# Optimization experiments

Hardware: AMD Instinct MI355X
Metric: run time of the kernel (lower is better)

## Reference

```python
import jax, jax.numpy as jnp
import numpy as np

B, N, N_MELS = 8, 4096, 64
DIM, LAYERS, HEADS = 256, 4, 4
DIM_HEAD = DIM // HEADS      # 64
INNER = HEADS * DIM_HEAD     # 256
NB_FEAT = 256                # random features
FF_MULT = 4                  # performer_pytorch FeedForward default


def _ortho_projection(rows, cols, rng):
    # gaussian_orthogonal_random_matrix, scaling=0 (performer_pytorch default)
    blocks = []
    for _ in range((rows + cols - 1) // cols):
        q, _ = np.linalg.qr(rng.standard_normal((cols, cols)))
        blocks.append(q.T)
    mat = np.concatenate(blocks)[:rows]
    multiplier = np.linalg.norm(rng.standard_normal((rows, cols)), axis=1)
    return (mat * multiplier[:, None]).astype(np.float32)


def setup_inputs() -> dict:
    rng = np.random.default_rng(0)
    def w(*s, scale=0.02):
        return jnp.asarray(rng.standard_normal(s).astype(np.float32) * scale)
    G2 = 2 * DIM * FF_MULT  # GLU projection width = 2048
    return {
        "x": jnp.asarray(rng.standard_normal((B, N, N_MELS)).astype(np.float32)),
        "proj_w": w(N_MELS, DIM), "proj_b": jnp.zeros((DIM,), jnp.float32),
        "ln1_g": jnp.ones((LAYERS, DIM), jnp.float32), "ln1_b": jnp.zeros((LAYERS, DIM), jnp.float32),
        "wq": w(LAYERS, DIM, INNER), "bq": jnp.zeros((LAYERS, INNER), jnp.float32),
        "wk": w(LAYERS, DIM, INNER), "bk": jnp.zeros((LAYERS, INNER), jnp.float32),
        "wv": w(LAYERS, DIM, INNER), "bv": jnp.zeros((LAYERS, INNER), jnp.float32),
        "wo": w(LAYERS, INNER, DIM), "bo": jnp.zeros((LAYERS, DIM), jnp.float32),
        "ln2_g": jnp.ones((LAYERS, DIM), jnp.float32), "ln2_b": jnp.zeros((LAYERS, DIM), jnp.float32),
        "w1": w(LAYERS, DIM, G2), "b1": jnp.zeros((LAYERS, G2), jnp.float32),
        "w2": w(LAYERS, DIM * FF_MULT, DIM), "b2": jnp.zeros((LAYERS, DIM), jnp.float32),
        "clf_w": w(DIM, 1), "clf_b": jnp.zeros((1,), jnp.float32),
        "proj_mat": jnp.asarray(_ortho_projection(NB_FEAT, DIM_HEAD, rng)),
    }


def _layer_norm(x, g, b, eps=1e-5):
    mu = jnp.mean(x, -1, keepdims=True)
    var = jnp.mean((x - mu) ** 2, -1, keepdims=True)
    return (x - mu) * jax.lax.rsqrt(var + eps) * g + b


def _softmax_kernel(data, proj, is_query, eps=1e-4):
    # FAVOR+ positive random features for softmax (performer_pytorch.softmax_kernel)
    dn = data.shape[-1] ** -0.25          # data_normalizer
    ratio = proj.shape[0] ** -0.5
    dd = jnp.einsum('bhnd,md->bhnm', data * dn, proj)
    diag = jnp.sum(data ** 2, -1, keepdims=True) * 0.5 * (dn ** 2)
    if is_query:
        m = jax.lax.stop_gradient(jnp.max(dd, axis=-1, keepdims=True))
    else:
        m = jax.lax.stop_gradient(jnp.max(dd))
    return ratio * (jnp.exp(dd - diag - m) + eps)


def _split_heads(t):
    b, n, _ = t.shape
    return t.reshape(b, n, HEADS, DIM_HEAD).transpose(0, 2, 1, 3)  # b h n d


def _forward(x, proj_w, proj_b, ln1_g, ln1_b, wq, bq, wk, bk, wv, bv, wo, bo,
             ln2_g, ln2_b, w1, b1, w2, b2, clf_w, clf_b, proj_mat):
    h = x @ proj_w + proj_b                       # [B, N, DIM]
    b, n = h.shape[0], h.shape[1]
    for l in range(LAYERS):
        # --- pre-LN self-attention (FAVOR+, non-causal) ---
        y = _layer_norm(h, ln1_g[l], ln1_b[l])
        q = _split_heads(y @ wq[l] + bq[l])
        k = _split_heads(y @ wk[l] + bk[l])
        v = _split_heads(y @ wv[l] + bv[l])
        qp = _softmax_kernel(q, proj_mat, is_query=True)    # [b,h,n,m]
        kp = _softmax_kernel(k, proj_mat, is_query=False)   # [b,h,n,m]
        d_inv = 1.0 / jnp.einsum('bhnm,bhm->bhn', qp, kp.sum(axis=2))
        ctx = jnp.einsum('bhnm,bhnd->bhmd', kp, v)          # [b,h,m,d]
        o = jnp.einsum('bhmd,bhnm,bhn->bhnd', ctx, qp, d_inv)
        o = o.transpose(0, 2, 1, 3).reshape(b, n, INNER)
        h = h + (o @ wo[l] + bo[l])
        # --- pre-LN GLU feed-forward ---
        y = _layer_norm(h, ln2_g[l], ln2_b[l])
        u = y @ w1[l] + b1[l]
        a, g = jnp.split(u, 2, axis=-1)
        h = h + (jax.nn.gelu(a, approximate=False) * g) @ w2[l] + b2[l]
    # clf: transpose + AdaptiveAvgPool1d(1) == mean over time, then Linear(dim,1)
    pooled = h.mean(axis=1)                       # [B, DIM]
    return (pooled @ clf_w + clf_b)[:, 0]         # [B]


def reference(x, proj_w, proj_b, ln1_g, ln1_b, wq, bq, wk, bk, wv, bv, wo, bo,
              ln2_g, ln2_b, w1, b1, w2, b2, clf_w, clf_b, proj_mat):
    return _forward(x, proj_w, proj_b, ln1_g, ln1_b, wq, bq, wk, bk, wv, bv,
                    wo, bo, ln2_g, ln2_b, w1, b1, w2, b2, clf_w, clf_b, proj_mat)
```

## Files before the change

kernel.cpp:

```cpp
#include <hip/hip_runtime.h>
#include <cstdint>
#include <cstddef>

constexpr float DN = 0.35355339059327373f;
constexpr float RATIO = 0.0625f;
constexpr float EPSF = 1e-4f;

typedef __attribute__((ext_vector_type(8))) short short8;
typedef __attribute__((ext_vector_type(4))) float f32x4;

constexpr size_t OFF_H     = 0;
constexpr size_t OFF_YS    = 33554432;
constexpr size_t OFF_WTS   = 50331648;
constexpr size_t OFF_QK    = 67108864;
constexpr size_t OFF_BIG   = 100663296;
constexpr size_t OFF_VT    = 167772160;
constexpr size_t OFF_CTXP  = 188743680;
constexpr size_t OFF_CTXTH = 199229440;
constexpr size_t OFF_CTXTL = 200540160;
constexpr size_t OFF_DIAGQ = 201850880;
constexpr size_t OFF_DIAGK = 202375168;
constexpr size_t OFF_GMAX  = 203423744;
constexpr size_t OFF_POOL  = 203424000;
constexpr size_t OFF_PMTH  = 207749376;
constexpr size_t OFF_PMTL  = 207782144;
constexpr size_t OFF_PWTH  = 207814912;
constexpr size_t OFF_PWTL  = 207847680;
constexpr size_t WS_BYTES  = 207880448;

constexpr size_t WQ_H = 0,       WQ_L = 65536;
constexpr size_t WK_H = 131072,  WK_L = 196608;
constexpr size_t WV_H = 262144,  WV_L = 327680;
constexpr size_t WO_H = 393216,  WO_L = 458752;
constexpr size_t W1_H = 524288,  W1_L = 1048576;
constexpr size_t W2_H = 1572864, W2_L = 1835008;

__device__ __forceinline__ unsigned fkey(float f) {
    unsigned u = __float_as_uint(f);
    return (u & 0x80000000u) ? ~u : (u | 0x80000000u);
}
__device__ __forceinline__ float funkey(unsigned k) {
    unsigned u = (k & 0x80000000u) ? (k ^ 0x80000000u) : ~k;
    return __uint_as_float(u);
}
__device__ __forceinline__ float gelu_exact(float x) {
    return 0.5f * x * (1.0f + erff(x * 0.70710678118654752f));
}
__device__ __forceinline__ void splitf(float x, unsigned short& h, unsigned short& l) {
    unsigned u = __float_as_uint(x);
    unsigned hv = (u + 0x7FFFu + ((u >> 16) & 1)) >> 16;
    h = (unsigned short)hv;
    float lo = x - __uint_as_float(hv << 16);
    unsigned u2 = __float_as_uint(lo);
    l = (unsigned short)((u2 + 0x7FFFu + ((u2 >> 16) & 1)) >> 16);
}
__device__ __forceinline__ unsigned short bf16rne(float x) {
    unsigned u = __float_as_uint(x);
    return (unsigned short)((u + 0x7FFFu + ((u >> 16) & 1)) >> 16);
}
__device__ __forceinline__ void xcd_swz(int& bx, int& by) {
    const int gx = gridDim.x;
    const int total = gx * gridDim.y;
    int flat = blockIdx.y * gx + blockIdx.x;
    flat = (flat & 7) * (total >> 3) + (flat >> 3);
    bx = flat % gx; by = flat / gx;
}

#if defined(__has_builtin)
#if __has_builtin(__builtin_amdgcn_global_load_lds)
#define HAVE_GLDS 1
#endif
#endif
__device__ __forceinline__ void glds16(const unsigned short* g, unsigned short* l) {
#ifdef HAVE_GLDS
    __builtin_amdgcn_global_load_lds(
        (const __attribute__((address_space(1))) unsigned int*)g,
        (__attribute__((address_space(3))) unsigned int*)l, 16, 0, 0);
#else
    *(uint4*)l = *(const uint4*)g;
#endif
}

__global__ void fill_sentinel(float* out, int n) {
    int i = threadIdx.x;
    if (i < n) out[i] = 12345.0f;
}
__global__ __launch_bounds__(256) void vt_init(unsigned short* __restrict__ vT, unsigned* __restrict__ gm) {
    int i = blockIdx.x * 256 + threadIdx.x;
    if (i < 4) gm[i] = 0u;
    const int bh = i >> 13;
    const int r = (i >> 9) & 15;
    const unsigned val = (r == 0) ? 0x3F803F80u : 0u;
    uint4 q; q.x = val; q.y = val; q.z = val; q.w = val;
    *(uint4*)(vT + ((size_t)bh * 80 + 64 + r) * 4096 + ((size_t)(i & 511) << 3)) = q;
}

__global__ __launch_bounds__(256) void split_scale(
    const float* __restrict__ src, unsigned short* __restrict__ hi,
    unsigned short* __restrict__ lo, int n, float scale)
{
    int i = blockIdx.x * 256 + threadIdx.x;
    if (i < n) {
        unsigned short h, l;
        splitf(src[i] * scale, h, l);
        hi[i] = h; lo[i] = l;
    }
}

__global__ __launch_bounds__(256) void splitT(
    const float* __restrict__ W, unsigned short* __restrict__ hi,
    unsigned short* __restrict__ lo, int kshift, int N)
{
    int i = blockIdx.x * 256 + threadIdx.x;
    int K = 1 << kshift;
    int n = i >> kshift, k = i & (K - 1);
    unsigned short h, l;
    splitf(W[(size_t)k * N + n], h, l);
    hi[i] = h; lo[i] = l;
}

__global__ __launch_bounds__(256) void split_weights(
    const float* __restrict__ wq, const float* __restrict__ wk,
    const float* __restrict__ wv, const float* __restrict__ wo,
    const float* __restrict__ w1, const float* __restrict__ w2,
    unsigned short* __restrict__ dst)
{
    const int i = blockIdx.x * 256 + threadIdx.x;
    const int lay = i >> 20;
    const int r = i & 1048575;
    float val; size_t oh, ol;
    if (r < 262144) {
        const int m = r >> 16, e = r & 65535;
        const int n = e >> 8, k = e & 255;
        const float* W = (m == 0 ? wq : m == 1 ? wk : m == 2 ? wv : wo);
        val = W[(size_t)lay * 65536 + k * 256 + n];
        oh = (size_t)lay * 2097152 + (size_t)m * 131072 + e;
        ol = oh + 65536;
    } else if (r < 786432) {
        const int e = r - 262144;
// ... 10 lines not shown
    }
    unsigned short h, l;
    splitf(val, h, l);
    dst[oh] = h; dst[ol] = l;
}

__global__ __launch_bounds__(256) void ln_bf16(
    const float* __restrict__ x, const float* __restrict__ g,
    const float* __restrict__ b, unsigned short* __restrict__ yhi)
{
    const int row = blockIdx.x * 4 + (threadIdx.x >> 6);
    const int lane = threadIdx.x & 63;
    float4 t = *(const float4*)&x[(size_t)row * 256 + lane * 4];
    float s = t.x + t.y + t.z + t.w;
#pragma unroll
    for (int sh = 1; sh < 64; sh <<= 1) s += __shfl_xor(s, sh);
    const float mu = s * (1.0f / 256.0f);
    const float dx = t.x - mu, dy = t.y - mu, dz = t.z - mu, dw = t.w - mu;
    float vv = dx * dx + dy * dy + dz * dz + dw * dw;
#pragma unroll
    for (int sh = 1; sh < 64; sh <<= 1) vv += __shfl_xor(vv, sh);
    const float rstd = rsqrtf(vv * (1.0f / 256.0f) + 1e-5f);
    float4 gv = *(const float4*)&g[lane * 4];
    float4 bv = *(const float4*)&b[lane * 4];
    unsigned short h0 = bf16rne(dx * rstd * gv.x + bv.x);
    unsigned short h1 = bf16rne(dy * rstd * gv.y + bv.y);
    unsigned short h2 = bf16rne(dz * rstd * gv.z + bv.z);
    unsigned short h3 = bf16rne(dw * rstd * gv.w + bv.w);
    uint2 ph;
    ph.x = (unsigned)h0 | ((unsigned)h1 << 16); ph.y = (unsigned)h2 | ((unsigned)h3 << 16);
    *(uint2*)&yhi[(size_t)row * 256 + lane * 4] = ph;
}

template<int EPI, bool ASPLIT, bool BSPLIT>
__global__ __launch_bounds__(256) void gemm_mf(
    const unsigned short* __restrict__ Ahi, const unsigned short* __restrict__ Alo, int lda,
    const unsigned short* __restrict__ Bhi, const unsigned short* __restrict__ Blo, int ldb,
    int K,
    const float* __restrict__ bias, const float* __restrict__ res,
    float* __restrict__ C, int ldc,
    unsigned short* __restrict__ Obf,
    const float* __restrict__ diag, unsigned* __restrict__ keys)
{
    constexpr int NP = (ASPLIT ? 2 : 1) + (BSPLIT ? 2 : 1);
    constexpr int PB = ASPLIT ? 2 : 1;
    constexpr int NEED = (EPI == 6 || EPI == 8) ? 16384 : 0;
    constexpr int LDSN = (NP * 8192 > NEED) ? NP * 8192 : NEED;
    __shared__ unsigned short lds[LDSN];
    __shared__ float red[4];
#define LX(p, h, r, c) lds[(p) * 8192 + (h) * 4096 + (r) * 32 + (c)]
    int bx, by; xcd_swz(bx, by);
    const int tid = threadIdx.x;
    const int m0 = by * 128, n0 = bx * 128;
    const int sr = tid >> 2, sc = (tid & 3) * 8;
    const unsigned short* ga_h = Ahi + (size_t)(m0 + sr) * lda + sc;
    const unsigned short* ga_l = ASPLIT ? (Alo + (size_t)(m0 + sr) * lda + sc) : nullptr;
    const unsigned short* gb_h = Bhi + (size_t)(n0 + sr) * ldb + sc;
    const unsigned short* gb_l = BSPLIT ? (Blo + (size_t)(n0 + sr) * ldb + sc) : nullptr;
    unsigned short* lp = lds + tid * 8;
    const int l = tid & 63, w = tid >> 6;
    const int wr = (w >> 1) * 64, wc = (w & 1) * 64;
    const int fr = l & 15, fq = l >> 4;

    f32x4 acc[4][4];
#pragma unroll
    for (int i = 0; i < 4; ++i)
#pragma unroll
        for (int j = 0; j < 4; ++j) acc[i][j] = (f32x4){0.f, 0.f, 0.f, 0.f};

    for (int k0 = 0; k0 < K; k0 += 64) {
        glds16(ga_h + k0, lp);
        glds16(ga_h + (size_t)64 * lda + k0, lp + 2048);
        glds16(ga_h + k0 + 32, lp + 4096);
        glds16(ga_h + (size_t)64 * lda + k0 + 32, lp + 6144);
        if (ASPLIT) {
            glds16(ga_l + k0, lp + 8192);
            glds16(ga_l + (size_t)64 * lda + k0, lp + 10240);
            glds16(ga_l + k0 + 32, lp + 12288);
            glds16(ga_l + (size_t)64 * lda + k0 + 32, lp + 14336);
        }
        glds16(gb_h + k0, lp + PB * 8192);
        glds16(gb_h + (size_t)64 * ldb + k0, lp + PB * 8192 + 2048);
        glds16(gb_h + k0 + 32, lp + PB * 8192 + 4096);
        glds16(gb_h + (size_t)64 * ldb + k0 + 32, lp + PB * 8192 + 6144);
        if (BSPLIT) {
            glds16(gb_l + k0, lp + (PB + 1) * 8192);
            glds16(gb_l + (size_t)64 * ldb + k0, lp + (PB + 1) * 8192 + 2048);
            glds16(gb_l + k0 + 32, lp + (PB + 1) * 8192 + 4096);
            glds16(gb_l + (size_t)64 * ldb + k0 + 32, lp + (PB + 1) * 8192 + 6144);
        }
        __syncthreads();
#pragma unroll
        for (int h2 = 0; h2 < 2; ++h2) {
            short8 ah[4], al[4];
#pragma unroll
            for (int mf = 0; mf < 4; ++mf) {
                ah[mf] = *(const short8*)&LX(0, h2, wr + mf * 16 + fr, fq * 8);
                if (ASPLIT) al[mf] = *(const short8*)&LX(1, h2, wr + mf * 16 + fr, fq * 8);
            }
#pragma unroll
            for (int nf = 0; nf < 4; ++nf) {
                short8 bh = *(const short8*)&LX(PB, h2, wc + nf * 16 + fr, fq * 8);
#pragma unroll
                for (int mf = 0; mf < 4; ++mf) {
                    acc[mf][nf] = __builtin_amdgcn_mfma_f32_16x16x32_bf16(ah[mf], bh, acc[mf][nf], 0, 0, 0);
                    if (ASPLIT)
                        acc[mf][nf] = __builtin_amdgcn_mfma_f32_16x16x32_bf16(al[mf], bh, acc[mf][nf], 0, 0, 0);
                }
                if (BSPLIT) {
                    short8 bl = *(const short8*)&LX(PB + 1, h2, wc + nf * 16 + fr, fq * 8);
#pragma unroll
                    for (int mf = 0; mf < 4; ++mf)
                        acc[mf][nf] = __builtin_amdgcn_mfma_f32_16x16x32_bf16(ah[mf], bl, acc[mf][nf], 0, 0, 0);
                }
            }
        }
        __syncthreads();
    }

    if constexpr (EPI == 4) {
        float m = -3.4e38f;
#pragma unroll
        for (int mf = 0; mf < 4; ++mf)
#pragma unroll
            for (int nf = 0; nf < 4; ++nf)
#pragma unroll
                for (int v = 0; v < 4; ++v) m = fmaxf(m, acc[mf][nf][v]);
#pragma unroll
        for (int s = 1; s < 64; s <<= 1) m = fmaxf(m, __shfl_xor(m, s));
        if (l == 0) red[w] = m;
        __syncthreads();
        if (tid == 0)
            atomicMax(keys, fkey(fmaxf(fmaxf(red[0], red[1]), fmaxf(red[2], red[3]))));
    } else if constexpr (EPI == 6) {
        const float Mg = funkey(*keys);
        unsigned short* tb = lds;
#pragma unroll
        for (int mf = 0; mf < 4; ++mf)
#pragma unroll
            for (int v = 0; v < 4; ++v) {
                const int rl = wr + mf * 16 + fq * 4 + v;
                const float dg = diag[m0 + rl] + Mg;
#pragma unroll
                for (int nf = 0; nf < 4; ++nf) {
                    const int cl = wc + nf * 16 + fr;
                    tb[rl * 128 + cl] = bf16rne(RATIO * (__expf(acc[mf][nf][v] - dg) + EPSF));
                }
            }
        __syncthreads();
        const int tokbase = m0 >> 2;
        const int b = tokbase >> 12, nib = tokbase & 4095;
        const int ml = tid & 127, g2 = tid >> 7;
#pragma unroll
        for (int hh2 = 0; hh2 < 2; ++hh2) {
            const int hh = g2 * 2 + hh2;
            unsigned short* dst = Obf + ((size_t)((b * 4 + hh) * 256 + n0 + ml)) * 4096 + nib;
#pragma unroll
            for (int qq = 0; qq < 4; ++qq) {
                uint4 qv;
                unsigned wv[4];
#pragma unroll
                for (int j = 0; j < 4; ++j) {
                    unsigned s0 = tb[((qq * 8 + j * 2 + 0) * 4 + hh) * 128 + ml];
                    unsigned s1 = tb[((qq * 8 + j * 2 + 1) * 4 + hh) * 128 + ml];
                    wv[j] = s0 | (s1 << 16);
                }
                qv.x = wv[0]; qv.y = wv[1]; qv.z = wv[2]; qv.w = wv[3];
                *(uint4*)(dst + qq * 8) = qv;
            }
        }
    } else if constexpr (EPI == 8) {
        unsigned short* tb = lds;
#pragma unroll
        for (int mf = 0; mf < 4; ++mf)
#pragma unroll
            for (int nf = 0; nf < 4; ++nf) {
                const int cl = wc + nf * 16 + fr;
                const float bb = bias[n0 + cl];
#pragma unroll
                for (int v = 0; v < 4; ++v) {
                    const int rl = wr + mf * 16 + fq * 4 + v;
                    tb[rl * 128 + cl] = bf16rne(acc[mf][nf][v] + bb);
                }
            }
        __syncthreads();
        const int b = m0 >> 12, nib = m0 & 4095;
        const int cl = tid & 127, half = tid >> 7;
        const int ch = n0 + cl, hh = ch >> 6, d = ch & 63;
        unsigned short* dst = Obf + ((size_t)((b * 4 + hh) * 80 + d)) * 4096 + nib + half * 64;
#pragma unroll
        for (int qq = 0; qq < 8; ++qq) {
            uint4 qv;
            unsigned wv[4];
#pragma unroll
            for (int j = 0; j < 4; ++j) {
                unsigned s0 = tb[(half * 64 + qq * 8 + j * 2 + 0) * 128 + cl];
                unsigned s1 = tb[(half * 64 + qq * 8 + j * 2 + 1) * 128 + cl];
                wv[j] = s0 | (s1 << 16);
            }
            qv.x = wv[0]; qv.y = wv[1]; qv.z = wv[2]; qv.w = wv[3];
            *(uint4*)(dst + qq * 8) = qv;
        }
    } else if constexpr (EPI == 2) {
        const int head = (n0 + wc) >> 6;
#pragma unroll
        for (int mf = 0; mf < 4; ++mf) {
            float sq[4] = {0.f, 0.f, 0.f, 0.f};
#pragma unroll
            for (int nf = 0; nf < 4; ++nf) {
                const int col = n0 + wc + nf * 16 + fr;
                const float bb = bias[col];
#pragma unroll
                for (int v = 0; v < 4; ++v) {
                    const int row = m0 + wr + mf * 16 + fq * 4 + v;
                    float val = acc[mf][nf][v] + bb;
                    Obf[(size_t)row * 256 + col] = bf16rne(val);
                    sq[v] += val * val;
                }
            }
#pragma unroll
            for (int v = 0; v < 4; ++v) {
                float s = sq[v];
                s += __shfl_xor(s, 1); s += __shfl_xor(s, 2);
                s += __shfl_xor(s, 4); s += __shfl_xor(s, 8);
                if (fr == 0)
                    ((float*)diag)[(size_t)(m0 + wr + mf * 16 + fq * 4 + v) * 4 + head] = s * 0.0625f;
            }
        }
    } else {
#pragma unroll
        for (int nf = 0; nf < 4; ++nf) {
            const int col = n0 + wc + nf * 16 + fr;
            float bb = 0.f;
            if (bias != nullptr) bb = bias[col];
#pragma unroll
            for (int mf = 0; mf < 4; ++mf) {
#pragma unroll
                for (int v = 0; v < 4; ++v) {
                    const int row = m0 + wr + mf * 16 + fq * 4 + v;
                    const size_t off = (size_t)row * ldc + col;
                    float val = acc[mf][nf][v] + bb;
                    if (EPI == 1) val += res[off];
                    C[off] = val;
                }
            }
        }
    }
#undef LX
}

__global__ __launch_bounds__(256) void gemm_glu(
    const unsigned short* __restrict__ Ahi,
    const unsigned short* __restrict__ Whi, const unsigned short* __restrict__ Wlo,
    const float* __restrict__ b1, unsigned short* __restrict__ Obf)
{
    __shared__ unsigned short ldsA[8192];
    __shared__ unsigned short ldsB[16384];
    int bx, by; xcd_swz(bx, by);
    const int tid = threadIdx.x;
    const int m0 = by * 128, p0 = bx * 64;
    const int sr = tid >> 2, sc = (tid & 3) * 8;
    const unsigned short* ga  = Ahi + (size_t)(m0 + sr) * 256 + sc;
    const unsigned short* gb0 = Whi + (size_t)(p0 + sr) * 256 + sc;
    const unsigned short* gb1 = Wlo + (size_t)(p0 + sr) * 256 + sc;
    const unsigned short* gb2 = Whi + (size_t)(1024 + p0 + sr) * 256 + sc;
    const unsigned short* gb3 = Wlo + (size_t)(1024 + p0 + sr) * 256 + sc;
    unsigned short* lpA = ldsA + tid * 8;
    unsigned short* lpB = ldsB + tid * 8;
    const int l = tid & 63, w = tid >> 6;
    const int wr = (w >> 1) * 64, wc = (w & 1) * 32;
    const int fr = l & 15, fq = l >> 4;

    f32x4 aa[4][2], ag[4][2];
#pragma unroll
    for (int i = 0; i < 4; ++i)
#pragma unroll
        for (int j = 0; j < 2; ++j) {
            aa[i][j] = (f32x4){0.f, 0.f, 0.f, 0.f};
            ag[i][j] = (f32x4){0.f, 0.f, 0.f, 0.f};
        }

    for (int k0 = 0; k0 < 256; k0 += 64) {
        glds16(ga + k0, lpA);
        glds16(ga + 64 * 256 + k0, lpA + 2048);
        glds16(ga + k0 + 32, lpA + 4096);
        glds16(ga + 64 * 256 + k0 + 32, lpA + 6144);
        glds16(gb0 + k0, lpB);
        glds16(gb0 + k0 + 32, lpB + 2048);
        glds16(gb1 + k0, lpB + 4096);
        glds16(gb1 + k0 + 32, lpB + 6144);
        glds16(gb2 + k0, lpB + 8192);
        glds16(gb2 + k0 + 32, lpB + 10240);
        glds16(gb3 + k0, lpB + 12288);
        glds16(gb3 + k0 + 32, lpB + 14336);
        __syncthreads();
#pragma unroll
        for (int h2 = 0; h2 < 2; ++h2) {
            short8 ah[4];
#pragma unroll
            for (int mf = 0; mf < 4; ++mf)
                ah[mf] = *(const short8*)&ldsA[h2 * 4096 + (wr + mf * 16 + fr) * 32 + fq * 8];
#pragma unroll
            for (int nf = 0; nf < 2; ++nf) {
                const int br_ = h2 * 2048 + (wc + nf * 16 + fr) * 32 + fq * 8;
                short8 bah = *(const short8*)&ldsB[br_];
                short8 bal = *(const short8*)&ldsB[4096 + br_];
                short8 bgh = *(const short8*)&ldsB[8192 + br_];
                short8 bgl = *(const short8*)&ldsB[12288 + br_];
#pragma unroll
                for (int mf = 0; mf < 4; ++mf) {
                    aa[mf][nf] = __builtin_amdgcn_mfma_f32_16x16x32_bf16(ah[mf], bah, aa[mf][nf], 0, 0, 0);
                    aa[mf][nf] = __builtin_amdgcn_mfma_f32_16x16x32_bf16(ah[mf], bal, aa[mf][nf], 0, 0, 0);
                    ag[mf][nf] = __builtin_amdgcn_mfma_f32_16x16x32_bf16(ah[mf], bgh, ag[mf][nf], 0, 0, 0);
                    ag[mf][nf] = __builtin_amdgcn_mfma_f32_16x16x32_bf16(ah[mf], bgl, ag[mf][nf], 0, 0, 0);
                }
            }
        }
        __syncthreads();
    }
#pragma unroll
    for (int nf = 0; nf < 2; ++nf) {
        const int ch = p0 + wc + nf * 16 + fr;
        const float ba = b1[ch], bg = b1[1024 + ch];
#pragma unroll
        for (int mf = 0; mf < 4; ++mf) {
#pragma unroll
            for (int v = 0; v < 4; ++v) {
                const int row = m0 + wr + mf * 16 + fq * 4 + v;
                float u = aa[mf][nf][v] + ba, g = ag[mf][nf][v] + bg;
                Obf[(size_t)row * 1024 + ch] = bf16rne(gelu_exact(u) * g);
            }
        }
    }
}

__global__ __launch_bounds__(256) void ctx_mfma(
    const unsigned short* __restrict__ kpT, const unsigned short* __restrict__ vT,
    float* __restrict__ ctxp)
{
    __shared__ unsigned short la[4096];
    __shared__ unsigned short lb[5120];
    int bx, by; xcd_swz(bx, by);
    const int bh = by, mt = bx & 3, kc = bx >> 2;
    const int tid = threadIdx.x;
    const int l = tid & 63, w = tid >> 6;
    const int wr = w * 16, fr = l & 15, fq = l >> 4;
    const int sr = tid >> 2, sc = (tid & 3) * 8;
    const unsigned short* ga  = kpT + ((size_t)bh * 256 + mt * 64 + sr) * 4096 + kc * 1024 + sc;
    const unsigned short* gb  = vT + ((size_t)bh * 80 + sr) * 4096 + kc * 1024 + sc;
    const unsigned short* gb2 = vT + ((size_t)bh * 80 + 64 + sr) * 4096 + kc * 1024 + sc;

    f32x4 acc[5];
#pragma unroll
    for (int j = 0; j < 5; ++j) acc[j] = (f32x4){0.f, 0.f, 0.f, 0.f};

    for (int k0 = 0; k0 < 1024; k0 += 64) {
        glds16(ga + k0, la + tid * 8);
        glds16(ga + k0 + 32, la + 2048 + tid * 8);
        glds16(gb + k0, lb + tid * 8);
        glds16(gb + k0 + 32, lb + 2560 + tid * 8);
        if (tid < 64) {
            glds16(gb2 + k0, lb + 2048 + tid * 8);
            glds16(gb2 + k0 + 32, lb + 2560 + 2048 + tid * 8);
        }
        __syncthreads();
#pragma unroll
        for (int h2 = 0; h2 < 2; ++h2) {
            short8 av = *(const short8*)&la[h2 * 2048 + (wr + fr) * 32 + fq * 8];
#pragma unroll
            for (int nf = 0; nf < 5; ++nf) {
                short8 bv = *(const short8*)&lb[h2 * 2560 + (nf * 16 + fr) * 32 + fq * 8];
                acc[nf] = __builtin_amdgcn_mfma_f32_16x16x32_bf16(av, bv, acc[nf], 0, 0, 0);
            }
        }
        __syncthreads();
    }
#pragma unroll
    for (int v = 0; v < 4; ++v) {
        const int row = mt * 64 + wr + fq * 4 + v;
#pragma unroll
        for (int nf = 0; nf < 5; ++nf)
            ctxp[((size_t)(kc * 32 + bh) * 256 + row) * 80 + nf * 16 + fr] = acc[nf][v];
    }
}

__global__ __launch_bounds__(256) void ctx_fix(
    const float* __restrict__ ctxp, unsigned short* __restrict__ cth,
    unsigned short* __restrict__ ctl)
{
    __shared__ float s[64][81];
    const int m0 = blockIdx.x * 64, bh = blockIdx.y;
    const int tid = threadIdx.x;
    for (int i = tid; i < 5120; i += 256) {
        const int ml = i / 80, dc = i % 80;
        float sum = 0.f;
#pragma unroll
        for (int kc = 0; kc < 4; ++kc)
            sum += ctxp[((size_t)(kc * 32 + bh) * 256 + m0 + ml) * 80 + dc];
        s[ml][dc] = sum;
    }
    __syncthreads();
    for (int i = tid; i < 5120; i += 256) {
        const int dc = i >> 6, ml = i & 63;
        unsigned short hh_, ll_;
        splitf(s[ml][dc], hh_, ll_);
        cth[((size_t)bh * 80 + dc) * 256 + m0 + ml] = hh_;
        ctl[((size_t)bh * 80 + dc) * 256 + m0 + ml] = ll_;
    }
}

__global__ __launch_bounds__(256) void qo_mfma(
    const unsigned short* __restrict__ qhi,
    const unsigned short* __restrict__ pmh, const unsigned short* __restrict__ pml,
    const unsigned short* __restrict__ cth, const unsigned short* __restrict__ ctl,
    const float* __restrict__ diagq, unsigned short* __restrict__ osh)
{
    __shared__ unsigned short lds[18432 + 5120];
    __shared__ float rmax4[64][4];
    int bx, by; xcd_swz(bx, by);
    const int bh = by, b = bh >> 2, hh = bh & 3;
    const int t0 = bx * 64;
    const int tid = threadIdx.x;
    const int l = tid & 63, w = tid >> 6;
    const int fr = l & 15, fq = l >> 4;

    const int wc1 = w * 64;
    f32x4 a1[4][4];
#pragma unroll
    for (int i = 0; i < 4; ++i)
#pragma unroll
        for (int j = 0; j < 4; ++j) a1[i][j] = (f32x4){0.f, 0.f, 0.f, 0.f};

    const unsigned short* gq = qhi + (size_t)(b * 4096 + t0) * 256 + hh * 64;
#pragma unroll
    for (int ks = 0; ks < 2; ++ks) {
        const int k0 = ks * 32;
        glds16(gq + (size_t)(tid >> 2) * 256 + k0 + (tid & 3) * 8, lds + tid * 8);
#pragma unroll
        for (int i2 = 0; i2 < 4; ++i2) {
            const int c = tid + i2 * 256;
            glds16(pmh + (size_t)(c >> 2) * 64 + k0 + (c & 3) * 8, lds + 2048 + c * 8);
            glds16(pml + (size_t)(c >> 2) * 64 + k0 + (c & 3) * 8, lds + 10240 + c * 8);
        }
        __syncthreads();
        short8 av[4];
#pragma unroll
        for (int mf = 0; mf < 4; ++mf)
            av[mf] = *(const short8*)&lds[(mf * 16 + fr) * 32 + fq * 8];
#pragma unroll
        for (int nf = 0; nf < 4; ++nf) {
            short8 bh_ = *(const short8*)&lds[2048 + (wc1 + nf * 16 + fr) * 32 + fq * 8];
            short8 bl_ = *(const short8*)&lds[10240 + (wc1 + nf * 16 + fr) * 32 + fq * 8];
#pragma unroll
            for (int mf = 0; mf < 4; ++mf) {
                a1[mf][nf] = __builtin_amdgcn_mfma_f32_16x16x32_bf16(av[mf], bh_, a1[mf][nf], 0, 0, 0);
                a1[mf][nf] = __builtin_amdgcn_mfma_f32_16x16x32_bf16(av[mf], bl_, a1[mf][nf], 0, 0, 0);
            }
        }
        __syncthreads();
    }
#pragma unroll
    for (int mf = 0; mf < 4; ++mf)
#pragma unroll
        for (int v = 0; v < 4; ++v) {
            float rm = a1[mf][0][v];
#pragma unroll
            for (int nf = 1; nf < 4; ++nf) rm = fmaxf(rm, a1[mf][nf][v]);
            rm = fmaxf(rm, __shfl_xor(rm, 1));
            rm = fmaxf(rm, __shfl_xor(rm, 2));
            rm = fmaxf(rm, __shfl_xor(rm, 4));
            rm = fmaxf(rm, __shfl_xor(rm, 8));
            if (fr == 0) rmax4[mf * 16 + fq * 4 + v][w] = rm;
        }
    __syncthreads();
#pragma unroll
    for (int mf = 0; mf < 4; ++mf)
#pragma unroll
        for (int v = 0; v < 4; ++v) {
            const int tok = mf * 16 + fq * 4 + v;
            const float dg = diagq[(size_t)(b * 4096 + t0 + tok) * 4 + hh]
                           + fmaxf(fmaxf(rmax4[tok][0], rmax4[tok][1]),
                                   fmaxf(rmax4[tok][2], rmax4[tok][3]));
#pragma unroll
            for (int nf = 0; nf < 4; ++nf) {
                const int m = wc1 + nf * 16 + fr;
                lds[tok * 256 + (m ^ ((tok & 7) << 3))] =
                    bf16rne(RATIO * (__expf(a1[mf][nf][v] - dg) + EPSF));
            }
        }
    __syncthreads();

    unsigned short* lds2 = lds + 18432;
    f32x4 a2[5];
#pragma unroll
    for (int j = 0; j < 5; ++j) a2[j] = (f32x4){0.f, 0.f, 0.f, 0.f};
    const size_t bbase = (size_t)bh * 80 * 256;

    for (int k0 = 0; k0 < 256; k0 += 32) {
        glds16(cth + bbase + (size_t)(tid >> 2) * 256 + k0 + (tid & 3) * 8, lds2 + tid * 8);
        glds16(ctl + bbase + (size_t)(tid >> 2) * 256 + k0 + (tid & 3) * 8, lds2 + 2560 + tid * 8);
        if (tid < 64) {
            const int c = 256 + tid;
            glds16(cth + bbase + (size_t)(c >> 2) * 256 + k0 + (c & 3) * 8, lds2 + c * 8);
            glds16(ctl + bbase + (size_t)(c >> 2) * 256 + k0 + (c & 3) * 8, lds2 + 2560 + c * 8);
        }
        __syncthreads();
        const int tok = w * 16 + fr;
        const int c = ((k0 >> 3) + fq) ^ (tok & 7);
        short8 av = *(const short8*)&lds[tok * 256 + c * 8];
#pragma unroll
        for (int nf = 0; nf < 5; ++nf) {
            const int off = (nf * 16 + fr) * 32 + fq * 8;
            short8 bvh = *(const short8*)&lds2[off];
            short8 bvl = *(const short8*)&lds2[2560 + off];
            a2[nf] = __builtin_amdgcn_mfma_f32_16x16x32_bf16(av, bvh, a2[nf], 0, 0, 0);
            a2[nf] = __builtin_amdgcn_mfma_f32_16x16x32_bf16(av, bvl, a2[nf], 0, 0, 0);
        }
        __syncthreads();
    }
#pragma unroll
    for (int v = 0; v < 4; ++v) {
        const float den = __shfl(a2[4][v], (int)(l & 48));
        const float dinv = 1.0f / den;
        const int tok = w * 16 + fq * 4 + v;
        const size_t obase = (size_t)(b * 4096 + t0 + tok) * 256 + hh * 64;
#pragma unroll
        for (int nf = 0; nf < 4; ++nf)
            osh[obase + nf * 16 + fr] = bf16rne(a2[nf][v] * dinv);
    }
}

__global__ __launch_bounds__(256) void pool1_kernel(const float* __restrict__ h, float* __restrict__ part)
{
    const int b = blockIdx.x >> 4, ch = blockIdx.x & 15;
    const int tid = threadIdx.x;
    float acc = 0.f;
    for (int n = 0; n < 256; ++n)
        acc += h[((size_t)(b * 4096 + ch * 256 + n)) * 256 + tid];
    part[(size_t)blockIdx.x * 256 + tid] = acc;
}

__global__ __launch_bounds__(256) void pool2_kernel(
    const float* __restrict__ part, const float* __restrict__ cw,
    const float* __restrict__ cb, float* __restrict__ out)
{
    const int b = blockIdx.x, tid = threadIdx.x;
    float acc = 0.f;
#pragma unroll
    for (int c = 0; c < 16; ++c) acc += part[(size_t)(b * 16 + c) * 256 + tid];
// ... 19 lines not shown
    const float* x     = (const float*)d_in[0];
    const float* projw = (const float*)d_in[1];
    const float* projb = (const float*)d_in[2];
    const float* ln1g  = (const float*)d_in[3];
    const float* ln1b  = (const float*)d_in[4];
    const float* wq    = (const float*)d_in[5];
    const float* bq    = (const float*)d_in[6];
    const float* wk    = (const float*)d_in[7];
    const float* bk    = (const float*)d_in[8];
    const float* wv    = (const float*)d_in[9];
    const float* bv    = (const float*)d_in[10];
    const float* wo    = (const float*)d_in[11];
    const float* bo    = (const float*)d_in[12];
    const float* ln2g  = (const float*)d_in[13];
    const float* ln2b  = (const float*)d_in[14];
    const float* w1    = (const float*)d_in[15];
    const float* b1    = (const float*)d_in[16];
    const float* w2    = (const float*)d_in[17];
    const float* b2    = (const float*)d_in[18];
    const float* clfw  = (const float*)d_in[19];
    const float* clfb  = (const float*)d_in[20];
    const float* projm = (const float*)d_in[21];

    char* WS = (char*)d_ws;
    float* h            = (float*)(WS + OFF_H);
    unsigned short* ysh = (unsigned short*)(WS + OFF_YS);
    unsigned short* wts = (unsigned short*)(WS + OFF_WTS);
    unsigned short* khi = (unsigned short*)(WS + OFF_QK);
    unsigned short* qhi = khi + 8388608;
    unsigned short* big = (unsigned short*)(WS + OFF_BIG);
    unsigned short* vT  = (unsigned short*)(WS + OFF_VT);
    float* ctxp         = (float*)(WS + OFF_CTXP);
    unsigned short* cth = (unsigned short*)(WS + OFF_CTXTH);
    unsigned short* ctl = (unsigned short*)(WS + OFF_CTXTL);
    float* diagq        = (float*)(WS + OFF_DIAGQ);
    float* diagk        = (float*)(WS + OFF_DIAGK);
    unsigned* gmax      = (unsigned*)(WS + OFF_GMAX);
    float* pool         = (float*)(WS + OFF_POOL);
    unsigned short* pmt_h = (unsigned short*)(WS + OFF_PMTH);
    unsigned short* pmt_l = (unsigned short*)(WS + OFF_PMTL);
    unsigned short* pwt_h = (unsigned short*)(WS + OFF_PWTH);
    unsigned short* pwt_l = (unsigned short*)(WS + OFF_PWTL);
    unsigned short* xsh = big;
    unsigned short* xsl = big + 2097152;
    unsigned short* kpT = big;
    unsigned short* ffb = big;
    unsigned short* osh = ysh;

    split_scale<<<8192, 256, 0, stream>>>(x, xsh, xsl, 2097152, 1.0f);
    splitT<<<64, 256, 0, stream>>>(projw, pwt_h, pwt_l, 6, 256);
    split_scale<<<64, 256, 0, stream>>>(projm, pmt_h, pmt_l, 16384, DN);
    vt_init<<<1024, 256, 0, stream>>>(vT, gmax);
    split_weights<<<16384, 256, 0, stream>>>(wq, wk, wv, wo, w1, w2, wts);
    gemm_mf<0, true, true><<<dim3(2, 256), 256, 0, stream>>>(xsh, xsl, 64, pwt_h, pwt_l, 64, 64,
        projb, nullptr, h, 256, nullptr, nullptr, nullptr);

    for (int l = 0; l < 4; ++l) {
        unsigned short* wl = wts + (size_t)l * 2097152;

        ln_bf16<<<8192, 256, 0, stream>>>(h, ln1g + l * 256, ln1b + l * 256, ysh);
        gemm_mf<8, false, true><<<dim3(2, 256), 256, 0, stream>>>(ysh, nullptr, 256,
            wl + WV_H, wl + WV_L, 256, 256, bv + l * 256, nullptr, nullptr, 256, vT, nullptr, nullptr);
        gemm_mf<2, false, true><<<dim3(2, 256), 256, 0, stream>>>(ysh, nullptr, 256,
            wl + WK_H, wl + WK_L, 256, 256, bk + l * 256, nullptr, nullptr, 256, khi, diagk, nullptr);
        gemm_mf<2, false, true><<<dim3(2, 256), 256, 0, stream>>>(ysh, nullptr, 256,
            wl + WQ_H, wl + WQ_L, 256, 256, bq + l * 256, nullptr, nullptr, 256, qhi, diagq, nullptr);
        gemm_mf<4, false, false><<<dim3(2, 1024), 256, 0, stream>>>(khi, nullptr, 64,
            pmt_h, nullptr, 64, 64, nullptr, nullptr, nullptr, 256, nullptr, nullptr, gmax + l);
        gemm_mf<6, false, true><<<dim3(2, 1024), 256, 0, stream>>>(khi, nullptr, 64,
            pmt_h, pmt_l, 64, 64, nullptr, nullptr, nullptr, 256, kpT, diagk, gmax + l);
        ctx_mfma<<<dim3(16, 32), 256, 0, stream>>>(kpT, vT, ctxp);
        ctx_fix<<<dim3(4, 32), 256, 0, stream>>>(ctxp, cth, ctl);
        qo_mfma<<<dim3(64, 32), 256, 0, stream>>>(qhi, pmt_h, pmt_l, cth, ctl, diagq, osh);
        gemm_mf<1, false, true><<<dim3(2, 256), 256, 0, stream>>>(osh, nullptr, 256,
            wl + WO_H, wl + WO_L, 256, 256, bo + l * 256, h, h, 256, nullptr, nullptr, nullptr);

        ln_bf16<<<8192, 256, 0, stream>>>(h, ln2g + l * 256, ln2b + l * 256, ysh);
        gemm_glu<<<dim3(16, 256), 256, 0, stream>>>(ysh, wl + W1_H, wl + W1_L,
            b1 + (size_t)l * 2048, ffb);
        gemm_mf<1, false, true><<<dim3(2, 256), 256, 0, stream>>>(ffb, nullptr, 1024,
            wl + W2_H, wl + W2_L, 1024, 1024, b2 + l * 256, h, h, 256, nullptr, nullptr, nullptr);
    }

    pool1_kernel<<<128, 256, 0, stream>>>(h, pool);
    pool2_kernel<<<8, 256, 0, stream>>>(pool, clfw, clfb, (float*)d_out);
}
```

Baseline: 1.424 ms.

## Use fp16 single-pass MFMA in FAVOR+ attention path and fuse QKV GEMMs

Switches the q/k/v, random-feature projection, context and output-attention operands from bf16 hi/lo split pairs to single fp16 values. This removes the low-part MFMA passes and the low-part loads in the kernel projection, ctx_fix and qo_mfma stages. The three separate Q, K and V projection launches are merged into one gemm_qkv kernel that selects its weights by block row. The trade-off is lower precision for the feature maps and context (fp16 mantissa instead of a split bf16 pair) and some fp16 range risk.

```diff
diff --git a/kernel.cpp b/kernel.cpp
--- a/kernel.cpp
+++ b/kernel.cpp
@@ -7,6 +7,7 @@
 constexpr float EPSF = 1e-4f;
 
 typedef __attribute__((ext_vector_type(8))) short short8;
+typedef __attribute__((ext_vector_type(8))) _Float16 half8;
 typedef __attribute__((ext_vector_type(4))) float f32x4;
 
 constexpr size_t OFF_H     = 0;
@@ -58,6 +59,17 @@
     unsigned u = __float_as_uint(x);
     return (unsigned short)((u + 0x7FFFu + ((u >> 16) & 1)) >> 16);
 }
+__device__ __forceinline__ unsigned short fp16rne(float x) {
+    return __builtin_bit_cast(unsigned short, (_Float16)x);
+}
+template<bool F16>
+__device__ __forceinline__ f32x4 mfma16(short8 a, short8 b, f32x4 c) {
+    if constexpr (F16)
+        return __builtin_amdgcn_mfma_f32_16x16x32_f16(
+            __builtin_bit_cast(half8, a), __builtin_bit_cast(half8, b), c, 0, 0, 0);
+    else
+        return __builtin_amdgcn_mfma_f32_16x16x32_bf16(a, b, c, 0, 0, 0);
+}
 __device__ __forceinline__ void xcd_swz(int& bx, int& by) {
     const int gx = gridDim.x;
     const int total = gx * gridDim.y;
@@ -90,7 +102,7 @@
     if (i < 4) gm[i] = 0u;
     const int bh = i >> 13;
     const int r = (i >> 9) & 15;
-    const unsigned val = (r == 0) ? 0x3F803F80u : 0u;
+    const unsigned val = (r == 0) ? 0x3C003C00u : 0u;
     uint4 q; q.x = val; q.y = val; q.z = val; q.w = val;
     *(uint4*)(vT + ((size_t)bh * 80 + 64 + r) * 4096 + ((size_t)(i & 511) << 3)) = q;
 }
@@ -105,6 +117,13 @@
         splitf(src[i] * scale, h, l);
         hi[i] = h; lo[i] = l;
     }
+}
+
+__global__ __launch_bounds__(256) void tofp16_scale(
+    const float* __restrict__ src, unsigned short* __restrict__ dst, int n, float scale)
+{
+    int i = blockIdx.x * 256 + threadIdx.x;
+    if (i < n) dst[i] = fp16rne(src[i] * scale);
 }
 
 __global__ __launch_bounds__(256) void splitT(
@@ -181,7 +200,7 @@
     *(uint2*)&yhi[(size_t)row * 256 + lane * 4] = ph;
 }
 
-template<int EPI, bool ASPLIT, bool BSPLIT>
+template<int EPI, bool ASPLIT, bool BSPLIT, bool F16>
 __global__ __launch_bounds__(256) void gemm_mf(
     const unsigned short* __restrict__ Ahi, const unsigned short* __restrict__ Alo, int lda,
     const unsigned short* __restrict__ Bhi, const unsigned short* __restrict__ Blo, int ldb,
@@ -193,7 +212,7 @@
 {
     constexpr int NP = (ASPLIT ? 2 : 1) + (BSPLIT ? 2 : 1);
     constexpr int PB = ASPLIT ? 2 : 1;
-    constexpr int NEED = (EPI == 6 || EPI == 8) ? 16384 : 0;
+    constexpr int NEED = (EPI == 6) ? 16384 : 0;
     constexpr int LDSN = (NP * 8192 > NEED) ? NP * 8192 : NEED;
     __shared__ unsigned short lds[LDSN];
     __shared__ float red[4];
@@ -252,15 +271,14 @@
                 short8 bh = *(const short8*)&LX(PB, h2, wc + nf * 16 + fr, fq * 8);
 #pragma unroll
                 for (int mf = 0; mf < 4; ++mf) {
-                    acc[mf][nf] = __builtin_amdgcn_mfma_f32_16x16x32_bf16(ah[mf], bh, acc[mf][nf], 0, 0, 0);
-                    if (ASPLIT)
-                        acc[mf][nf] = __builtin_amdgcn_mfma_f32_16x16x32_bf16(al[mf], bh, acc[mf][nf], 0, 0, 0);
+                    acc[mf][nf] = mfma16<F16>(ah[mf], bh, acc[mf][nf]);
+                    if (ASPLIT) acc[mf][nf] = mfma16<F16>(al[mf], bh, acc[mf][nf]);
                 }
                 if (BSPLIT) {
                     short8 bl = *(const short8*)&LX(PB + 1, h2, wc + nf * 16 + fr, fq * 8);
 #pragma unroll
                     for (int mf = 0; mf < 4; ++mf)
-                        acc[mf][nf] = __builtin_amdgcn_mfma_f32_16x16x32_bf16(ah[mf], bl, acc[mf][nf], 0, 0, 0);
+                        acc[mf][nf] = mfma16<F16>(ah[mf], bl, acc[mf][nf]);
                 }
             }
         }
@@ -293,7 +311,8 @@
 #pragma unroll
                 for (int nf = 0; nf < 4; ++nf) {
                     const int cl = wc + nf * 16 + fr;
-                    tb[rl * 128 + cl] = bf16rne(RATIO * (__expf(acc[mf][nf][v] - dg) + EPSF));
+                    const float kv = RATIO * (__expf(acc[mf][nf][v] - dg) + EPSF);
+                    tb[rl * 128 + cl] = F16 ? fp16rne(kv) : bf16rne(kv);
                 }
             }
         __syncthreads();
@@ -318,64 +337,6 @@
                 *(uint4*)(dst + qq * 8) = qv;
             }
         }
-    } else if constexpr (EPI == 8) {
-        unsigned short* tb = lds;
-#pragma unroll
-        for (int mf = 0; mf < 4; ++mf)
-#pragma unroll
-            for (int nf = 0; nf < 4; ++nf) {
-                const int cl = wc + nf * 16 + fr;
-                const float bb = bias[n0 + cl];
-#pragma unroll
-                for (int v = 0; v < 4; ++v) {
-                    const int rl = wr + mf * 16 + fq * 4 + v;
-                    tb[rl * 128 + cl] = bf16rne(acc[mf][nf][v] + bb);
-                }
-            }
-        __syncthreads();
-        const int b = m0 >> 12, nib = m0 & 4095;
-        const int cl = tid & 127, half = tid >> 7;
-        const int ch = n0 + cl, hh = ch >> 6, d = ch & 63;
-        unsigned short* dst = Obf + ((size_t)((b * 4 + hh) * 80 + d)) * 4096 + nib + half * 64;
-#pragma unroll
-        for (int qq = 0; qq < 8; ++qq) {
-            uint4 qv;
-            unsigned wv[4];
-#pragma unroll
-            for (int j = 0; j < 4; ++j) {
-                unsigned s0 = tb[(half * 64 + qq * 8 + j * 2 + 0) * 128 + cl];
-                unsigned s1 = tb[(half * 64 + qq * 8 + j * 2 + 1) * 128 + cl];
-                wv[j] = s0 | (s1 << 16);
-            }
-            qv.x = wv[0]; qv.y = wv[1]; qv.z = wv[2]; qv.w = wv[3];
-            *(uint4*)(dst + qq * 8) = qv;
-        }
-    } else if constexpr (EPI == 2) {
-        const int head = (n0 + wc) >> 6;
-#pragma unroll
-        for (int mf = 0; mf < 4; ++mf) {
-            float sq[4] = {0.f, 0.f, 0.f, 0.f};
-#pragma unroll
-            for (int nf = 0; nf < 4; ++nf) {
-                const int col = n0 + wc + nf * 16 + fr;
-                const float bb = bias[col];
-#pragma unroll
-                for (int v = 0; v < 4; ++v) {
-                    const int row = m0 + wr + mf * 16 + fq * 4 + v;
-                    float val = acc[mf][nf][v] + bb;
-                    Obf[(size_t)row * 256 + col] = bf16rne(val);
-                    sq[v] += val * val;
-                }
-            }
-#pragma unroll
-            for (int v = 0; v < 4; ++v) {
-                float s = sq[v];
-                s += __shfl_xor(s, 1); s += __shfl_xor(s, 2);
-                s += __shfl_xor(s, 4); s += __shfl_xor(s, 8);
-                if (fr == 0)
-                    ((float*)diag)[(size_t)(m0 + wr + mf * 16 + fq * 4 + v) * 4 + head] = s * 0.0625f;
-            }
-        }
     } else {
 #pragma unroll
         for (int nf = 0; nf < 4; ++nf) {
@@ -396,6 +357,132 @@
         }
     }
 #undef LX
+}
+
+__global__ __launch_bounds__(256) void gemm_qkv(
+    const unsigned short* __restrict__ A, const unsigned short* __restrict__ wl,
+    const float* __restrict__ bq, const float* __restrict__ bk, const float* __restrict__ bv,
+    unsigned short* __restrict__ vT, unsigned short* __restrict__ khi,
+    unsigned short* __restrict__ qhi, float* __restrict__ diagq, float* __restrict__ diagk)
+{
+    __shared__ unsigned short lds[24576];
+    int bx, by; xcd_swz(bx, by);
+    const int sel = by >> 8;
+    const int m0 = (by & 255) * 128, n0 = bx * 128;
+    const unsigned short* Bh = wl + (sel == 0 ? WV_H : sel == 1 ? WK_H : WQ_H);
+    const unsigned short* Bl = wl + (sel == 0 ? WV_L : sel == 1 ? WK_L : WQ_L);
+    const float* bias = (sel == 0 ? bv : sel == 1 ? bk : bq);
+    const int tid = threadIdx.x;
+    const int sr = tid >> 2, sc = (tid & 3) * 8;
+    const unsigned short* ga_h = A + (size_t)(m0 + sr) * 256 + sc;
+    const unsigned short* gb_h = Bh + (size_t)(n0 + sr) * 256 + sc;
+    const unsigned short* gb_l = Bl + (size_t)(n0 + sr) * 256 + sc;
+    unsigned short* lp = lds + tid * 8;
+    const int l = tid & 63, w = tid >> 6;
+    const int wr = (w >> 1) * 64, wc = (w & 1) * 64;
+    const int fr = l & 15, fq = l >> 4;
+
+    f32x4 acc[4][4];
+#pragma unroll
+    for (int i = 0; i < 4; ++i)
+#pragma unroll
+        for (int j = 0; j < 4; ++j) acc[i][j] = (f32x4){0.f, 0.f, 0.f, 0.f};
+
+    for (int k0 = 0; k0 < 256; k0 += 64) {
+        glds16(ga_h + k0, lp);
+        glds16(ga_h + (size_t)64 * 256 + k0, lp + 2048);
+        glds16(ga_h + k0 + 32, lp + 4096);
+        glds16(ga_h + (size_t)64 * 256 + k0 + 32, lp + 6144);
+        glds16(gb_h + k0, lp + 8192);
+        glds16(gb_h + (size_t)64 * 256 + k0, lp + 10240);
+        glds16(gb_h + k0 + 32, lp + 12288);
+        glds16(gb_h + (size_t)64 * 256 + k0 + 32, lp + 14336);
+        glds16(gb_l + k0, lp + 16384);
+        glds16(gb_l + (size_t)64 * 256 + k0, lp + 18432);
+        glds16(gb_l + k0 + 32, lp + 20480);
+        glds16(gb_l + (size_t)64 * 256 + k0 + 32, lp + 22528);
+        __syncthreads();
+#pragma unroll
+        for (int h2 = 0; h2 < 2; ++h2) {
+            short8 ah[4];
+#pragma unroll
+            for (int mf = 0; mf < 4; ++mf)
+                ah[mf] = *(const short8*)&lds[h2 * 4096 + (wr + mf * 16 + fr) * 32 + fq * 8];
+#pragma unroll
+            for (int nf = 0; nf < 4; ++nf) {
+                short8 bh = *(const short8*)&lds[8192 + h2 * 4096 + (wc + nf * 16 + fr) * 32 + fq * 8];
+                short8 bl = *(const short8*)&lds[16384 + h2 * 4096 + (wc + nf * 16 + fr) * 32 + fq * 8];
+#pragma unroll
+                for (int mf = 0; mf < 4; ++mf) {
+                    acc[mf][nf] = mfma16<false>(ah[mf], bh, acc[mf][nf]);
+                    acc[mf][nf] = mfma16<false>(ah[mf], bl, acc[mf][nf]);
+                }
+            }
+        }
+        __syncthreads();
+    }
+
+    if (sel == 0) {
+        unsigned short* tb = lds;
+#pragma unroll
+        for (int mf = 0; mf < 4; ++mf)
+#pragma unroll
+            for (int nf = 0; nf < 4; ++nf) {
+                const int cl = wc + nf * 16 + fr;
+                const float bb = bias[n0 + cl];
+#pragma unroll
+                for (int v = 0; v < 4; ++v) {
+                    const int rl = wr + mf * 16 + fq * 4 + v;
+                    tb[rl * 128 + cl] = fp16rne(acc[mf][nf][v] + bb);
+                }
+            }
+        __syncthreads();
+        const int b = m0 >> 12, nib = m0 & 4095;
+        const int cl = tid & 127, half = tid >> 7;
+        const int ch = n0 + cl, hh = ch >> 6, d = ch & 63;
+        unsigned short* dst = vT + ((size_t)((b * 4 + hh) * 80 + d)) * 4096 + nib + half * 64;
+#pragma unroll
+        for (int qq = 0; qq < 8; ++qq) {
+            uint4 qv;
+            unsigned wv[4];
+#pragma unroll
+            for (int j = 0; j < 4; ++j) {
+                unsigned s0 = tb[(half * 64 + qq * 8 + j * 2 + 0) * 128 + cl];
+                unsigned s1 = tb[(half * 64 + qq * 8 + j * 2 + 1) * 128 + cl];
+                wv[j] = s0 | (s1 << 16);
+            }
+            qv.x = wv[0]; qv.y = wv[1]; qv.z = wv[2]; qv.w = wv[3];
+            *(uint4*)(dst + qq * 8) = qv;
+        }
+    } else {
+        float* diag = (sel == 1 ? diagk : diagq);
+        unsigned short* Obf = (sel == 1 ? khi : qhi);
+        const int head = (n0 + wc) >> 6;
+#pragma unroll
+        for (int mf = 0; mf < 4; ++mf) {
+            float sq[4] = {0.f, 0.f, 0.f, 0.f};
+#pragma unroll
+            for (int nf = 0; nf < 4; ++nf) {
+                const int col = n0 + wc + nf * 16 + fr;
+                const float bb = bias[col];
+#pragma unroll
+                for (int v = 0; v < 4; ++v) {
+                    const int row = m0 + wr + mf * 16 + fq * 4 + v;
+                    float val = acc[mf][nf][v] + bb;
+                    Obf[(size_t)row * 256 + col] = fp16rne(val);
+                    sq[v] += val * val;
+                }
+            }
+#pragma unroll
+            for (int v = 0; v < 4; ++v) {
+                float s = sq[v];
+                s += __shfl_xor(s, 1); s += __shfl_xor(s, 2);
+                s += __shfl_xor(s, 4); s += __shfl_xor(s, 8);
+                if (fr == 0)
+                    diag[(size_t)(m0 + wr + mf * 16 + fq * 4 + v) * 4 + head] = s * 0.0625f;
+            }
+        }
+    }
 }
 
 __global__ __launch_bounds__(256) void gemm_glu(
@@ -458,10 +545,10 @@
                 short8 bgl = *(const short8*)&ldsB[12288 + br_];
 #pragma unroll
                 for (int mf = 0; mf < 4; ++mf) {
-                    aa[mf][nf] = __builtin_amdgcn_mfma_f32_16x16x32_bf16(ah[mf], bah, aa[mf][nf], 0, 0, 0);
-                    aa[mf][nf] = __builtin_amdgcn_mfma_f32_16x16x32_bf16(ah[mf], bal, aa[mf][nf], 0, 0, 0);
-                    ag[mf][nf] = __builtin_amdgcn_mfma_f32_16x16x32_bf16(ah[mf], bgh, ag[mf][nf], 0, 0, 0);
-                    ag[mf][nf] = __builtin_amdgcn_mfma_f32_16x16x32_bf16(ah[mf], bgl, ag[mf][nf], 0, 0, 0);
+                    aa[mf][nf] = mfma16<false>(ah[mf], bah, aa[mf][nf]);
+                    aa[mf][nf] = mfma16<false>(ah[mf], bal, aa[mf][nf]);
+                    ag[mf][nf] = mfma16<false>(ah[mf], bgh, ag[mf][nf]);
+                    ag[mf][nf] = mfma16<false>(ah[mf], bgl, ag[mf][nf]);
                 }
             }
         }
@@ -519,7 +606,7 @@
 #pragma unroll
             for (int nf = 0; nf < 5; ++nf) {
                 short8 bv = *(const short8*)&lb[h2 * 2560 + (nf * 16 + fr) * 32 + fq * 8];
-                acc[nf] = __builtin_amdgcn_mfma_f32_16x16x32_bf16(av, bv, acc[nf], 0, 0, 0);
+                acc[nf] = mfma16<true>(av, bv, acc[nf]);
             }
         }
         __syncthreads();
@@ -534,8 +621,7 @@
 }
 
 __global__ __launch_bounds__(256) void ctx_fix(
-    const float* __restrict__ ctxp, unsigned short* __restrict__ cth,
-    unsigned short* __restrict__ ctl)
+    const float* __restrict__ ctxp, unsigned short* __restrict__ cth)
 {
     __shared__ float s[64][81];
     const int m0 = blockIdx.x * 64, bh = blockIdx.y;
@@ -551,20 +637,16 @@
     __syncthreads();
     for (int i = tid; i < 5120; i += 256) {
         const int dc = i >> 6, ml = i & 63;
-        unsigned short hh_, ll_;
-        splitf(s[ml][dc], hh_, ll_);
-        cth[((size_t)bh * 80 + dc) * 256 + m0 + ml] = hh_;
-        ctl[((size_t)bh * 80 + dc) * 256 + m0 + ml] = ll_;
+        cth[((size_t)bh * 80 + dc) * 256 + m0 + ml] = fp16rne(s[ml][dc]);
     }
 }
 
 __global__ __launch_bounds__(256) void qo_mfma(
-    const unsigned short* __restrict__ qhi,
-    const unsigned short* __restrict__ pmh, const unsigned short* __restrict__ pml,
-    const unsigned short* __restrict__ cth, const unsigned short* __restrict__ ctl,
-    const float* __restrict__ diagq, unsigned short* __restrict__ osh)
-{
-    __shared__ unsigned short lds[18432 + 5120];
+    const unsigned short* __restrict__ qhi, const unsigned short* __restrict__ pmh,
+    const unsigned short* __restrict__ cth, const float* __restrict__ diagq,
+    unsigned short* __restrict__ osh)
+{
+    __shared__ unsigned short lds[16384 + 2560];
     __shared__ float rmax4[64][4];
     int bx, by; xcd_swz(bx, by);
     const int bh = by, b = bh >> 2, hh = bh & 3;
@@ -589,7 +671,6 @@
         for (int i2 = 0; i2 < 4; ++i2) {
             const int c = tid + i2 * 256;
             glds16(pmh + (size_t)(c >> 2) * 64 + k0 + (c & 3) * 8, lds + 2048 + c * 8);
-            glds16(pml + (size_t)(c >> 2) * 64 + k0 + (c & 3) * 8, lds + 10240 + c * 8);
         }
         __syncthreads();
         short8 av[4];
@@ -599,12 +680,9 @@
 #pragma unroll
         for (int nf = 0; nf < 4; ++nf) {
             short8 bh_ = *(const short8*)&lds[2048 + (wc1 + nf * 16 + fr) * 32 + fq * 8];
-            short8 bl_ = *(const short8*)&lds[10240 + (wc1 + nf * 16 + fr) * 32 + fq * 8];
-#pragma unroll
-            for (int mf = 0; mf < 4; ++mf) {
-                a1[mf][nf] = __builtin_amdgcn_mfma_f32_16x16x32_bf16(av[mf], bh_, a1[mf][nf], 0, 0, 0);
-                a1[mf][nf] = __builtin_amdgcn_mfma_f32_16x16x32_bf16(av[mf], bl_, a1[mf][nf], 0, 0, 0);
-            }
+#pragma unroll
+            for (int mf = 0; mf < 4; ++mf)
+                a1[mf][nf] = mfma16<true>(av[mf], bh_, a1[mf][nf]);
         }
         __syncthreads();
     }
@@ -634,12 +712,12 @@
             for (int nf = 0; nf < 4; ++nf) {
                 const int m = wc1 + nf * 16 + fr;
                 lds[tok * 256 + (m ^ ((tok & 7) << 3))] =
-                    bf16rne(RATIO * (__expf(a1[mf][nf][v] - dg) + EPSF));
+                    fp16rne(RATIO * (__expf(a1[mf][nf][v] - dg) + EPSF));
             }
         }
     __syncthreads();
 
-    unsigned short* lds2 = lds + 18432;
+    unsigned short* lds2 = lds + 16384;
     f32x4 a2[5];
 #pragma unroll
     for (int j = 0; j < 5; ++j) a2[j] = (f32x4){0.f, 0.f, 0.f, 0.f};
@@ -647,11 +725,9 @@
 
     for (int k0 = 0; k0 < 256; k0 += 32) {
         glds16(cth + bbase + (size_t)(tid >> 2) * 256 + k0 + (tid & 3) * 8, lds2 + tid * 8);
-        glds16(ctl + bbase + (size_t)(tid >> 2) * 256 + k0 + (tid & 3) * 8, lds2 + 2560 + tid * 8);
         if (tid < 64) {
             const int c = 256 + tid;
             glds16(cth + bbase + (size_t)(c >> 2) * 256 + k0 + (c & 3) * 8, lds2 + c * 8);
-            glds16(ctl + bbase + (size_t)(c >> 2) * 256 + k0 + (c & 3) * 8, lds2 + 2560 + c * 8);
         }
         __syncthreads();
         const int tok = w * 16 + fr;
@@ -659,11 +735,8 @@
         short8 av = *(const short8*)&lds[tok * 256 + c * 8];
 #pragma unroll
         for (int nf = 0; nf < 5; ++nf) {
-            const int off = (nf * 16 + fr) * 32 + fq * 8;
-            short8 bvh = *(const short8*)&lds2[off];
-            short8 bvl = *(const short8*)&lds2[2560 + off];
-            a2[nf] = __builtin_amdgcn_mfma_f32_16x16x32_bf16(av, bvh, a2[nf], 0, 0, 0);
-            a2[nf] = __builtin_amdgcn_mfma_f32_16x16x32_bf16(av, bvl, a2[nf], 0, 0, 0);
+            short8 bvh = *(const short8*)&lds2[(nf * 16 + fr) * 32 + fq * 8];
+            a2[nf] = mfma16<true>(av, bvh, a2[nf]);
         }
         __syncthreads();
     }
@@ -749,13 +822,11 @@
     unsigned short* vT  = (unsigned short*)(WS + OFF_VT);
     float* ctxp         = (float*)(WS + OFF_CTXP);
     unsigned short* cth = (unsigned short*)(WS + OFF_CTXTH);
-    unsigned short* ctl = (unsigned short*)(WS + OFF_CTXTL);
     float* diagq        = (float*)(WS + OFF_DIAGQ);
     float* diagk        = (float*)(WS + OFF_DIAGK);
     unsigned* gmax      = (unsigned*)(WS + OFF_GMAX);
     float* pool         = (float*)(WS + OFF_POOL);
     unsigned short* pmt_h = (unsigned short*)(WS + OFF_PMTH);
-    unsigned short* pmt_l = (unsigned short*)(WS + OFF_PMTL);
     unsigned short* pwt_h = (unsigned short*)(WS + OFF_PWTH);
     unsigned short* pwt_l = (unsigned short*)(WS + OFF_PWTL);
     unsigned short* xsh = big;
@@ -766,36 +837,32 @@
 
     split_scale<<<8192, 256, 0, stream>>>(x, xsh, xsl, 2097152, 1.0f);
     splitT<<<64, 256, 0, stream>>>(projw, pwt_h, pwt_l, 6, 256);
-    split_scale<<<64, 256, 0, stream>>>(projm, pmt_h, pmt_l, 16384, DN);
+    tofp16_scale<<<64, 256, 0, stream>>>(projm, pmt_h, 16384, DN);
     vt_init<<<1024, 256, 0, stream>>>(vT, gmax);
     split_weights<<<16384, 256, 0, stream>>>(wq, wk, wv, wo, w1, w2, wts);
-    gemm_mf<0, true, true><<<dim3(2, 256), 256, 0, stream>>>(xsh, xsl, 64, pwt_h, pwt_l, 64, 64,
-        projb, nullptr, h, 256, nullptr, nullptr, nullptr);
+    gemm_mf<0, true, true, false><<<dim3(2, 256), 256, 0, stream>>>(xsh, xsl, 64,
+        pwt_h, pwt_l, 64, 64, projb, nullptr, h, 256, nullptr, nullptr, nullptr);
 
     for (int l = 0; l < 4; ++l) {
         unsigned short* wl = wts + (size_t)l * 2097152;
 
         ln_bf16<<<8192, 256, 0, stream>>>(h, ln1g + l * 256, ln1b + l * 256, ysh);
-        gemm_mf<8, false, true><<<dim3(2, 256), 256, 0, stream>>>(ysh, nullptr, 256,
-            wl + WV_H, wl + WV_L, 256, 256, bv + l * 256, nullptr, nullptr, 256, vT, nullptr, nullptr);
-        gemm_mf<2, false, true><<<dim3(2, 256), 256, 0, stream>>>(ysh, nullptr, 256,
-            wl + WK_H, wl + WK_L, 256, 256, bk + l * 256, nullptr, nullptr, 256, khi, diagk, nullptr);
-        gemm_mf<2, false, true><<<dim3(2, 256), 256, 0, stream>>>(ysh, nullptr, 256,
-            wl + WQ_H, wl + WQ_L, 256, 256, bq + l * 256, nullptr, nullptr, 256, qhi, diagq, nullptr);
-        gemm_mf<4, false, false><<<dim3(2, 1024), 256, 0, stream>>>(khi, nullptr, 64,
+        gemm_qkv<<<dim3(2, 768), 256, 0, stream>>>(ysh, wl,
+            bq + l * 256, bk + l * 256, bv + l * 256, vT, khi, qhi, diagq, diagk);
+        gemm_mf<4, false, false, true><<<dim3(2, 1024), 256, 0, stream>>>(khi, nullptr, 64,
             pmt_h, nullptr, 64, 64, nullptr, nullptr, nullptr, 256, nullptr, nullptr, gmax + l);
-        gemm_mf<6, false, true><<<dim3(2, 1024), 256, 0, stream>>>(khi, nullptr, 64,
-            pmt_h, pmt_l, 64, 64, nullptr, nullptr, nullptr, 256, kpT, diagk, gmax + l);
+        gemm_mf<6, false, false, true><<<dim3(2, 1024), 256, 0, stream>>>(khi, nullptr, 64,
+            pmt_h, nullptr, 64, 64, nullptr, nullptr, nullptr, 256, kpT, diagk, gmax + l);
         ctx_mfma<<<dim3(16, 32), 256, 0, stream>>>(kpT, vT, ctxp);
-        ctx_fix<<<dim3(4, 32), 256, 0, stream>>>(ctxp, cth, ctl);
-        qo_mfma<<<dim3(64, 32), 256, 0, stream>>>(qhi, pmt_h, pmt_l, cth, ctl, diagq, osh);
-        gemm_mf<1, false, true><<<dim3(2, 256), 256, 0, stream>>>(osh, nullptr, 256,
+        ctx_fix<<<dim3(4, 32), 256, 0, stream>>>(ctxp, cth);
+        qo_mfma<<<dim3(64, 32), 256, 0, stream>>>(qhi, pmt_h, cth, diagq, osh);
+        gemm_mf<1, false, true, false><<<dim3(2, 256), 256, 0, stream>>>(osh, nullptr, 256,
             wl + WO_H, wl + WO_L, 256, 256, bo + l * 256, h, h, 256, nullptr, nullptr, nullptr);
 
         ln_bf16<<<8192, 256, 0, stream>>>(h, ln2g + l * 256, ln2b + l * 256, ysh);
         gemm_glu<<<dim3(16, 256), 256, 0, stream>>>(ysh, wl + W1_H, wl + W1_L,
             b1 + (size_t)l * 2048, ffb);
-        gemm_mf<1, false, true><<<dim3(2, 256), 256, 0, stream>>>(ffb, nullptr, 1024,
+        gemm_mf<1, false, true, false><<<dim3(2, 256), 256, 0, stream>>>(ffb, nullptr, 1024,
             wl + W2_H, wl + W2_L, 1024, 1024, b2 + l * 256, h, h, 256, nullptr, nullptr, nullptr);
     }
 
```

Measured after the change: 1.341 ms. -5.8%, faster.
